# Kernel tuning notes

Hardware: AMD Instinct MI355X
Metric: run time of the kernel (lower is better)

Reference implementation:

```python
import jax, jax.numpy as jnp
import numpy as np

N_NODES = 50000
N_EDGES = 800000
HIDDEN = 128
NUM_BASIS = 32
CUTOFF = 5.0


def setup_inputs() -> dict:
    key = jax.random.key(0)
    ks = jax.random.split(key, 9)
    node_features = jax.random.normal(ks[0], (N_NODES, HIDDEN), dtype=jnp.float32)
    positions = jax.random.normal(ks[1], (N_NODES, 3), dtype=jnp.float32)
    edge_index = jax.random.randint(ks[2], (2, N_EDGES), 0, N_NODES)
    edge_in = 2 * HIDDEN + NUM_BASIS
    W1 = jax.random.normal(ks[3], (edge_in, HIDDEN), dtype=jnp.float32) * (edge_in ** -0.5)
    b1 = jnp.zeros((HIDDEN,), dtype=jnp.float32)
    W2 = jax.random.normal(ks[4], (HIDDEN, HIDDEN), dtype=jnp.float32) * (HIDDEN ** -0.5)
    b2 = jnp.zeros((HIDDEN,), dtype=jnp.float32)
    Wo = jax.random.normal(ks[5], (HIDDEN, HIDDEN), dtype=jnp.float32) * (HIDDEN ** -0.5)
    bo = jnp.zeros((HIDDEN,), dtype=jnp.float32)
    return dict(node_features=node_features, positions=positions, edge_index=edge_index,
                W1=W1, b1=b1, W2=W2, b2=b2, Wo=Wo, bo=bo)


def reference(node_features, positions, edge_index, W1, b1, W2, b2, Wo, bo):
    n_nodes = node_features.shape[0]
    # Gaussian radial basis (fixed buffers)
    centers = jnp.linspace(0.0, CUTOFF, NUM_BASIS)  # [NB]
    width = 0.5 * (centers[1] - centers[0] + 0.01)
    src, dst = edge_index[0], edge_index[1]
    rel = positions[dst] - positions[src]                       # [E,3]
    dist = jnp.linalg.norm(rel, axis=-1)                        # [E]
    d = jnp.minimum(dist, CUTOFF)
    rbf = jnp.exp(-0.5 * ((d[:, None] - centers) / width) ** 2)  # [E,NB]
    # edge message: concat(src feats, dst feats, rbf) -> 2-layer SiLU MLP
    msg = jnp.concatenate([node_features[src], node_features[dst], rbf], axis=-1)  # [E,2H+NB]
    h = jax.nn.silu(msg @ W1 + b1) @ W2 + b2                    # [E,H]
    # scatter-add to destination nodes + degree normalization
    updates = jax.ops.segment_sum(h, dst, num_segments=n_nodes)          # [N,H]
    degree = jax.ops.segment_sum(jnp.ones_like(dist), dst, num_segments=n_nodes)
    updates = updates / jnp.maximum(degree, 1.0)[:, None]
    return updates @ Wo + bo
```

## Files before the change

kernel.cpp:

```cpp
#include <hip/hip_runtime.h>

#define NN 50000
#define NE 800000
#define HID 128
#define NB 32
#define SCAN_B 196

typedef short short8 __attribute__((ext_vector_type(8)));
typedef float f32x4 __attribute__((ext_vector_type(4)));

static __device__ __forceinline__ short f2bf(float x) {
    unsigned int u = __float_as_uint(x);
    unsigned int r = (u + 0x7fffu + ((u >> 16) & 1u)) >> 16;
    return (short)r;
}

static __device__ __forceinline__ unsigned int addpack(unsigned int a, unsigned int b) {
    float lo = __uint_as_float(a << 16) + __uint_as_float(b << 16);
    float hi = __uint_as_float(a & 0xffff0000u) + __uint_as_float(b & 0xffff0000u);
    return ((unsigned int)(unsigned short)f2bf(hi) << 16) | (unsigned short)f2bf(lo);
}

__global__ void fused_prep(const int* __restrict__ dstI, int* __restrict__ counts,
                           const float* __restrict__ W1, const float* __restrict__ W2,
                           const float* __restrict__ Wo,
                           short* __restrict__ W1aT, short* __restrict__ W1bT,
                           short* __restrict__ W1cT, short* __restrict__ W2t,
                           short* __restrict__ Wot) {
    int b = blockIdx.x;
    if (b < 3125) {
        int e = b * 256 + threadIdx.x;
        atomicAdd(&counts[dstI[e]], 1);
    } else {
        int t = (b - 3125) * 256 + threadIdx.x;
        if (t < 16384) {
            int n = t >> 7, k = t & 127;
            W1aT[t] = f2bf(W1[k * HID + n]);
        } else if ((t -= 16384) < 16384) {
            int n = t >> 7, k = t & 127;
            W1bT[t] = f2bf(W1[(k + 128) * HID + n]);
        } else if ((t -= 16384) < 4096) {
            int n = t >> 5, k = t & 31;
            W1cT[t] = f2bf(W1[(k + 256) * HID + n]);
        } else if ((t -= 4096) < 16384) {
            int n = t >> 7, k = t & 127;
            W2t[t] = f2bf(W2[k * HID + n]);
        } else if ((t -= 16384) < 16384) {
            int n = t >> 7, k = t & 127;
            Wot[t] = f2bf(Wo[k * HID + n]);
        }
    }
}

__global__ void k_scan1(const int* __restrict__ counts, int* __restrict__ scanEx,
                        int* __restrict__ blockSum) {
    __shared__ int s[256];
    int t = threadIdx.x, idx = blockIdx.x * 256 + t;
    int v = counts[idx];
    s[t] = v; __syncthreads();
    #pragma unroll
    for (int off = 1; off < 256; off <<= 1) {
        int x = (t >= off) ? s[t - off] : 0;
        __syncthreads();
        s[t] += x;
        __syncthreads();
    }
    scanEx[idx] = s[t] - v;
    if (t == 255) blockSum[blockIdx.x] = s[255];
}

__global__ void k_scan2(const int* __restrict__ blockSum, int* __restrict__ blockBase) {
    __shared__ int s[256];
    int t = threadIdx.x;
    int v = (t < SCAN_B) ? blockSum[t] : 0;
    s[t] = v; __syncthreads();
    #pragma unroll
    for (int off = 1; off < 256; off <<= 1) {
        int x = (t >= off) ? s[t - off] : 0;
        __syncthreads();
        s[t] += x;
        __syncthreads();
    }
    blockBase[t] = s[t] - v;
}

__global__ void k_scan3(const int* __restrict__ scanEx, const int* __restrict__ blockBase,
                        int* __restrict__ cur) {
    int idx = blockIdx.x * 256 + threadIdx.x;
    cur[idx] = scanEx[idx] + blockBase[blockIdx.x];
}

__global__ void k_permute(const int* __restrict__ src, const int* __restrict__ dst,
                          int* __restrict__ cur, int2* __restrict__ edgeS) {
    int e = blockIdx.x * 256 + threadIdx.x;
    int s = src[e];
    int d = dst[e];
    int r = atomicAdd(&cur[d], 1);
    edgeS[r] = make_int2(s, d);
}

__global__ void sd_kernel(const float* __restrict__ nf,
                          const short* __restrict__ W1aT, const short* __restrict__ W1bT,
                          short* __restrict__ Sg, short* __restrict__ Dg) {
    __shared__ short As[64 * 136];
    const int tid  = threadIdx.x;
    const int wave = tid >> 6;
    const int lane = tid & 63;
    const int quad = lane >> 4;
    const int l15  = lane & 15;
    const int n0   = blockIdx.x * 64;

    {
        int row = tid >> 2, pt = tid & 3;
        int node = min(n0 + row, NN - 1);
        const float4* p = (const float4*)(nf + (size_t)node * HID + pt * 32);
        #pragma unroll
        for (int j = 0; j < 4; ++j) {
            float4 w0 = p[j * 2], w1 = p[j * 2 + 1];
            short8 o;
            o[0] = f2bf(w0.x); o[1] = f2bf(w0.y); o[2] = f2bf(w0.z); o[3] = f2bf(w0.w);
            o[4] = f2bf(w1.x); o[5] = f2bf(w1.y); o[6] = f2bf(w1.z); o[7] = f2bf(w1.w);
            *(short8*)(As + row * 136 + pt * 32 + j * 8) = o;
        }
    }
    __syncthreads();

    f32x4 aS[4][2], aD[4][2];
    #pragma unroll
    for (int mt = 0; mt < 4; ++mt)
        #pragma unroll
        for (int nt = 0; nt < 2; ++nt) {
            aS[mt][nt] = (f32x4){0.f, 0.f, 0.f, 0.f};
            aD[mt][nt] = (f32x4){0.f, 0.f, 0.f, 0.f};
        }

    #pragma unroll
    for (int kk = 0; kk < 4; ++kk) {
        int ko = kk * 32 + quad * 8;
        short8 a[4];
        #pragma unroll
        for (int mt = 0; mt < 4; ++mt)
            a[mt] = *(const short8*)(As + (mt * 16 + l15) * 136 + ko);
        #pragma unroll
        for (int nt = 0; nt < 2; ++nt) {
            int n = wave * 32 + nt * 16 + l15;
            short8 bS = *(const short8*)(W1aT + n * HID + ko);
            short8 bD = *(const short8*)(W1bT + n * HID + ko);
            #pragma unroll
            for (int mt = 0; mt < 4; ++mt) {
                aS[mt][nt] = __builtin_amdgcn_mfma_f32_16x16x32_bf16(a[mt], bS, aS[mt][nt], 0, 0, 0);
                aD[mt][nt] = __builtin_amdgcn_mfma_f32_16x16x32_bf16(a[mt], bD, aD[mt][nt], 0, 0, 0);
            }
        }
    }

    #pragma unroll
    for (int nt = 0; nt < 2; ++nt) {
        int col = wave * 32 + nt * 16 + l15;
        #pragma unroll
        for (int mt = 0; mt < 4; ++mt) {
            #pragma unroll
            for (int r = 0; r < 4; ++r) {
                int node = n0 + mt * 16 + quad * 4 + r;
                if (node < NN) {
                    Sg[(size_t)node * HID + col] = f2bf(aS[mt][nt][r]);
                    Dg[(size_t)node * HID + col] = f2bf(aD[mt][nt][r]);
                }
            }
        }
    }
}

__launch_bounds__(512, 6)
__global__ void edge_kernel(const short* __restrict__ Sg,
                            const short* __restrict__ Dg,
                            const float* __restrict__ pos,
                            const int2* __restrict__ edgeS,
                            const short* __restrict__ W1cT,
                            const float* __restrict__ b1,
                            const short* __restrict__ W2t,
                            const float* __restrict__ b2,
                            float* __restrict__ upd) {
    __shared__ char buf[49152];
    __shared__ int  dn_sh[128];
    short* PRE = (short*)buf;
    short* R   = (short*)(buf + 34816);
    short* Ps  = (short*)buf;
    float* UfT = (float*)buf;

    const int tid  = threadIdx.x;
    const int wave = tid >> 6;
    const int lane = tid & 63;
    const int quad = lane >> 4;
    const int l15  = lane & 15;
    const int mg   = wave >> 2;
    const int nsl  = wave & 3;
    const int e0   = blockIdx.x * 128;

    {
        int es = tid >> 2, pt = tid & 3;
        int2 sd = edgeS[e0 + es];
        int s = sd.x, d = sd.y;
        const int4* sp = (const int4*)(Sg + (size_t)s * HID + pt * 32);
        const int4* dp = (const int4*)(Dg + (size_t)d * HID + pt * 32);
        int4* op = (int4*)(PRE + es * 136 + pt * 32);
        #pragma unroll
        for (int j = 0; j < 4; ++j) {
            int4 a = sp[j], b = dp[j];
            int4 o;
            o.x = addpack(a.x, b.x);
            o.y = addpack(a.y, b.y);
            o.z = addpack(a.z, b.z);
            o.w = addpack(a.w, b.w);
            op[j] = o;
        }
        if (pt == 0) dn_sh[es] = d;
        float dx = pos[d * 3 + 0] - pos[s * 3 + 0];
        float dy = pos[d * 3 + 1] - pos[s * 3 + 1];
        float dz = pos[d * 3 + 2] - pos[s * 3 + 2];
        float dd = fminf(sqrtf(dx * dx + dy * dy + dz * dz), 5.0f);
        const float step  = 5.0f / 31.0f;
        const float width = 0.5f * (step + 0.01f);
        const float coef  = -0.5f / (width * width);
        short8 r;
        #pragma unroll
        for (int j = 0; j < 8; ++j) {
            float c = step * (float)(pt * 8 + j);
            float t = dd - c;
            r[j] = f2bf(__expf(coef * t * t));
        }
        *(short8*)(R + es * 56 + pt * 8) = r;
    }
    __syncthreads();

    f32x4 acc[4][2];
    #pragma unroll
    for (int mt = 0; mt < 4; ++mt)
        #pragma unroll
        for (int nt = 0; nt < 2; ++nt) acc[mt][nt] = (f32x4){0.f, 0.f, 0.f, 0.f};
    {
        int ko = quad * 8;
        short8 a[4];
        #pragma unroll
        for (int mt = 0; mt < 4; ++mt)
            a[mt] = *(const short8*)(R + (mg * 64 + mt * 16 + l15) * 56 + ko);
        #pragma unroll
        for (int nt = 0; nt < 2; ++nt) {
            int n = nsl * 32 + nt * 16 + l15;
            short8 b = *(const short8*)(W1cT + n * NB + ko);
            #pragma unroll
            for (int mt = 0; mt < 4; ++mt)
                acc[mt][nt] = __builtin_amdgcn_mfma_f32_16x16x32_bf16(a[mt], b, acc[mt][nt], 0, 0, 0);
        }
    }

    {
        float b1c[2] = { b1[nsl * 32 + l15], b1[nsl * 32 + 16 + l15] };
        const unsigned short* PREu = (const unsigned short*)PRE;
        #pragma unroll
        for (int nt = 0; nt < 2; ++nt) {
            int col = nsl * 32 + nt * 16 + l15;
            #pragma unroll
            for (int mt = 0; mt < 4; ++mt) {
                #pragma unroll
                for (int r = 0; r < 4; ++r) {
                    int row = mg * 64 + mt * 16 + quad * 4 + r;
                    float pre = __uint_as_float((unsigned int)PREu[row * 136 + col] << 16);
                    float x = acc[mt][nt][r] + pre + b1c[nt];
                    float p = x / (1.0f + __expf(-x));
                    Ps[row * 136 + col] = f2bf(p);
                }
            }
        }
    }
    __syncthreads();

    f32x4 acc2[4][2];
    #pragma unroll
    for (int mt = 0; mt < 4; ++mt)
        #pragma unroll
        for (int nt = 0; nt < 2; ++nt) acc2[mt][nt] = (f32x4){0.f, 0.f, 0.f, 0.f};

    #pragma unroll
    for (int kk = 0; kk < 4; ++kk) {
        int ko = kk * 32 + quad * 8;
        short8 a[4];
        #pragma unroll
        for (int mt = 0; mt < 4; ++mt)
            a[mt] = *(const short8*)(Ps + (mg * 64 + mt * 16 + l15) * 136 + ko);
        #pragma unroll
        for (int nt = 0; nt < 2; ++nt) {
            int n = nsl * 32 + nt * 16 + l15;
            short8 b = *(const short8*)(W2t + n * HID + ko);
            #pragma unroll
            for (int mt = 0; mt < 4; ++mt)
                acc2[mt][nt] = __builtin_amdgcn_mfma_f32_16x16x32_bf16(a[mt], b, acc2[mt][nt], 0, 0, 0);
        }
    }
    __syncthreads();

    float b2c[2] = { b2[nsl * 32 + l15], b2[nsl * 32 + 16 + l15] };
    #pragma unroll
    for (int h = 0; h < 2; ++h) {
        if (mg == h) {
            #pragma unroll
            for (int nt = 0; nt < 2; ++nt) {
                int col = nsl * 32 + nt * 16 + l15;
                #pragma unroll
                for (int mt = 0; mt < 4; ++mt) {
                    f32x4 v;
                    #pragma unroll
                    for (int r = 0; r < 4; ++r) v[r] = acc2[mt][nt][r] + b2c[nt];
                    *(f32x4*)(UfT + col * 68 + mt * 16 + quad * 4) = v;
                }
            }
        }
        __syncthreads();
        {
            int col = tid & 127;
            int seg = tid >> 7;
            int rb  = h * 64 + seg * 16;
            const float* cp = UfT + col * 68 + seg * 16;
            f32x4 vv[4];
            #pragma unroll
            for (int j = 0; j < 4; ++j) vv[j] = *(const f32x4*)(cp + j * 4);
            int rnode = dn_sh[rb];
            float run = 0.0f;
            #pragma unroll
            for (int i = 0; i < 16; ++i) {
                int node = dn_sh[rb + i];
                float v = vv[i >> 2][i & 3];
                if (node != rnode) {
                    atomicAdd(upd + (size_t)rnode * HID + col, run);
                    rnode = node;
                    run = v;
                } else {
                    run += v;
                }
            }
            atomicAdd(upd + (size_t)rnode * HID + col, run);
        }
        __syncthreads();
    }
}

__launch_bounds__(256, 4)
__global__ void out_kernel(float* __restrict__ out,
                           const int* __restrict__ counts,
                           const short* __restrict__ Wot,
                           const float* __restrict__ bo) {
    __shared__ short A2[64 * 136];

    const int tid  = threadIdx.x;
    const int wave = tid >> 6;
    const int lane = tid & 63;
    const int quad = lane >> 4;
    const int l15  = lane & 15;
    const int n0   = blockIdx.x * 64;

    {
        int row = tid >> 2, pt = tid & 3;
        int node = n0 + row;
        if (node < NN) {
            float inv = 1.0f / fmaxf((float)counts[node], 1.0f);
            const float4* p = (const float4*)(out + (size_t)node * HID + pt * 32);
            #pragma unroll
            for (int j = 0; j < 4; ++j) {
                float4 w0 = p[j * 2], w1 = p[j * 2 + 1];
                short8 o;
                o[0] = f2bf(w0.x * inv); o[1] = f2bf(w0.y * inv);
                o[2] = f2bf(w0.z * inv); o[3] = f2bf(w0.w * inv);
                o[4] = f2bf(w1.x * inv); o[5] = f2bf(w1.y * inv);
                o[6] = f2bf(w1.z * inv); o[7] = f2bf(w1.w * inv);
                *(short8*)(A2 + row * 136 + pt * 32 + j * 8) = o;
            }
        } else {
            short8 z = (short8){0, 0, 0, 0, 0, 0, 0, 0};
            #pragma unroll
            for (int j = 0; j < 4; ++j)
                *(short8*)(A2 + row * 136 + pt * 32 + j * 8) = z;
        }
    }
    __syncthreads();

    f32x4 acc[4][2];
    #pragma unroll
    for (int mt = 0; mt < 4; ++mt)
        #pragma unroll
        for (int nt = 0; nt < 2; ++nt) acc[mt][nt] = (f32x4){0.f, 0.f, 0.f, 0.f};

    #pragma unroll
    for (int kk = 0; kk < 4; ++kk) {
        int ko = kk * 32 + quad * 8;
        short8 a[4];
        #pragma unroll
        for (int mt = 0; mt < 4; ++mt)
            a[mt] = *(const short8*)(A2 + (mt * 16 + l15) * 136 + ko);
        #pragma unroll
        for (int nt = 0; nt < 2; ++nt) {
            int n = wave * 32 + nt * 16 + l15;
            short8 b = *(const short8*)(Wot + n * HID + ko);
            #pragma unroll
            for (int mt = 0; mt < 4; ++mt)
                acc[mt][nt] = __builtin_amdgcn_mfma_f32_16x16x32_bf16(a[mt], b, acc[mt][nt], 0, 0, 0);
        }
    }
    __syncthreads();

    #pragma unroll
    for (int nt = 0; nt < 2; ++nt) {
        int col = wave * 32 + nt * 16 + l15;
        float bias = bo[col];
        #pragma unroll
        for (int mt = 0; mt < 4; ++mt) {
            #pragma unroll
            for (int r = 0; r < 4; ++r) {
                int row = mt * 16 + quad * 4 + r;
                int node = n0 + row;
                if (node < NN)
                    out[(size_t)node * HID + col] = acc[mt][nt][r] + bias;
            }
        }
    }
}

extern "C" void kernel_launch(void* const* d_in, const int* in_sizes, int n_in,
                              void* d_out, int out_size, void* d_ws, size_t ws_size,
                              hipStream_t stream) {
    const float* nf  = (const float*)d_in[0];
    const float* pos = (const float*)d_in[1];
    const int*   ei  = (const int*)d_in[2];
    const float* W1  = (const float*)d_in[3];
    const float* b1  = (const float*)d_in[4];
    const float* W2  = (const float*)d_in[5];
    const float* b2  = (const float*)d_in[6];
    const float* Wo  = (const float*)d_in[7];
    const float* bo  = (const float*)d_in[8];
    float* out = (float*)d_out;

    char* ws = (char*)d_ws;
    short* W1aT     = (short*)(ws);
    short* W1bT     = (short*)(ws + 32768);
    short* W1cT     = (short*)(ws + 65536);
    short* W2t      = (short*)(ws + 73728);
    short* Wot      = (short*)(ws + 106496);
    int*   counts   = (int*)(ws + 139264);
    int*   scanEx   = (int*)(ws + 339968);
    int*   blockSum = (int*)(ws + 540672);
    int*   blockBase= (int*)(ws + 541696);
    int*   cur      = (int*)(ws + 542720);
    int2*  edgeS    = (int2*)(ws + 743424);
    short* Sg       = (short*)(ws + 7143424);
    short* Dg       = (short*)(ws + 19943424);

    hipMemsetAsync(out, 0, (size_t)NN * HID * sizeof(float), stream);
    hipMemsetAsync(counts, 0, 200704, stream);

    fused_prep<<<3397, 256, 0, stream>>>(ei + NE, counts, W1, W2, Wo,
                                         W1aT, W1bT, W1cT, W2t, Wot);
    k_scan1<<<SCAN_B, 256, 0, stream>>>(counts, scanEx, blockSum);
    k_scan2<<<1, 256, 0, stream>>>(blockSum, blockBase);
    k_scan3<<<SCAN_B, 256, 0, stream>>>(scanEx, blockBase, cur);
    k_permute<<<3125, 256, 0, stream>>>(ei, ei + NE, cur, edgeS);
    sd_kernel<<<(NN + 63) / 64, 256, 0, stream>>>(nf, W1aT, W1bT, Sg, Dg);
    edge_kernel<<<NE / 128, 512, 0, stream>>>(Sg, Dg, pos, edgeS,
                                              W1cT, b1, W2t, b2, out);
    out_kernel<<<(NN + 63) / 64, 256, 0, stream>>>(out, counts, Wot, bo);
}
```

Baseline: 345.8 us.

## Fuse edge MLP, scatter and output GEMM into per-node-block kernel

Replaces the edge-parallel kernel, which used global atomics into the output, and the separate output kernel with one kernel that owns 16 destination nodes per block. Each block walks its CSR edge range in tiles of 64, runs the MLP, and accumulates into shared memory, then applies degree normalization and the Wo projection in place. The two scan tail kernels are merged, the output memset is dropped, and scanEx now aliases the Sg buffer. The aim is to remove global float atomics and an extra round trip of the update tensor, at the cost of load imbalance across blocks and partially filled edge tiles.

```diff
diff --git a/kernel.cpp b/kernel.cpp
--- a/kernel.cpp
+++ b/kernel.cpp
@@ -5,6 +5,8 @@
 #define HID 128
 #define NB 32
 #define SCAN_B 196
+#define NPB 16
+#define ET 64
 
 typedef short short8 __attribute__((ext_vector_type(8)));
 typedef float f32x4 __attribute__((ext_vector_type(4)));
@@ -14,11 +16,8 @@
     unsigned int r = (u + 0x7fffu + ((u >> 16) & 1u)) >> 16;
     return (short)r;
 }
-
-static __device__ __forceinline__ unsigned int addpack(unsigned int a, unsigned int b) {
-    float lo = __uint_as_float(a << 16) + __uint_as_float(b << 16);
-    float hi = __uint_as_float(a & 0xffff0000u) + __uint_as_float(b & 0xffff0000u);
-    return ((unsigned int)(unsigned short)f2bf(hi) << 16) | (unsigned short)f2bf(lo);
+static __device__ __forceinline__ float bf2f(unsigned short s) {
+    return __uint_as_float(((unsigned int)s) << 16);
 }
 
 __global__ void fused_prep(const int* __restrict__ dstI, int* __restrict__ counts,
@@ -69,25 +68,21 @@
     if (t == 255) blockSum[blockIdx.x] = s[255];
 }
 
-__global__ void k_scan2(const int* __restrict__ blockSum, int* __restrict__ blockBase) {
+__global__ void k_scan23(const int* __restrict__ scanEx, const int* __restrict__ blockSum,
+                         int* __restrict__ nodeBase, int* __restrict__ cur) {
     __shared__ int s[256];
-    int t = threadIdx.x;
-    int v = (t < SCAN_B) ? blockSum[t] : 0;
-    s[t] = v; __syncthreads();
-    #pragma unroll
-    for (int off = 1; off < 256; off <<= 1) {
-        int x = (t >= off) ? s[t - off] : 0;
-        __syncthreads();
-        s[t] += x;
-        __syncthreads();
-    }
-    blockBase[t] = s[t] - v;
-}
-
-__global__ void k_scan3(const int* __restrict__ scanEx, const int* __restrict__ blockBase,
-                        int* __restrict__ cur) {
-    int idx = blockIdx.x * 256 + threadIdx.x;
-    cur[idx] = scanEx[idx] + blockBase[blockIdx.x];
+    int t = threadIdx.x, b = blockIdx.x;
+    s[t] = (t < b) ? blockSum[t] : 0;
+    __syncthreads();
+    #pragma unroll
+    for (int off = 128; off > 0; off >>= 1) {
+        if (t < off) s[t] += s[t + off];
+        __syncthreads();
+    }
+    int idx = b * 256 + t;
+    int val = scanEx[idx] + s[0];
+    nodeBase[idx] = val;
+    cur[idx] = val;
 }
 
 __global__ void k_permute(const int* __restrict__ src, const int* __restrict__ dst,
@@ -171,255 +166,208 @@
     }
 }
 
-__launch_bounds__(512, 6)
-__global__ void edge_kernel(const short* __restrict__ Sg,
-                            const short* __restrict__ Dg,
-                            const float* __restrict__ pos,
-                            const int2* __restrict__ edgeS,
-                            const short* __restrict__ W1cT,
-                            const float* __restrict__ b1,
-                            const short* __restrict__ W2t,
-                            const float* __restrict__ b2,
-                            float* __restrict__ upd) {
-    __shared__ char buf[49152];
-    __shared__ int  dn_sh[128];
-    short* PRE = (short*)buf;
-    short* R   = (short*)(buf + 34816);
-    short* Ps  = (short*)buf;
-    float* UfT = (float*)buf;
+__launch_bounds__(256, 4)
+__global__ void edge_node(const short* __restrict__ Sg,
+                          const short* __restrict__ Dg,
+                          const float* __restrict__ pos,
+                          const int2* __restrict__ edgeS,
+                          const int* __restrict__ nodeBase,
+                          const int* __restrict__ counts,
+                          const short* __restrict__ W1cT,
+                          const float* __restrict__ b1,
+                          const short* __restrict__ W2t,
+                          const float* __restrict__ b2,
+                          const short* __restrict__ Wot,
+                          const float* __restrict__ bo,
+                          float* __restrict__ out) {
+    __shared__ float accL[17 * 132];
+    __shared__ short Ps[ET * 136];
+    __shared__ short R[ET * 56];
+    __shared__ short Dl[17 * 128];
+    __shared__ int   dn_sh[ET];
+    __shared__ float inv_sh[NPB];
 
     const int tid  = threadIdx.x;
-    const int wave = tid >> 6;
     const int lane = tid & 63;
+    const int nsl  = tid >> 6;
     const int quad = lane >> 4;
     const int l15  = lane & 15;
-    const int mg   = wave >> 2;
-    const int nsl  = wave & 3;
-    const int e0   = blockIdx.x * 128;
-
+    const int n0   = blockIdx.x * NPB;
+
+    for (int i = tid; i < 17 * 132; i += 256) accL[i] = 0.f;
     {
-        int es = tid >> 2, pt = tid & 3;
-        int2 sd = edgeS[e0 + es];
-        int s = sd.x, d = sd.y;
-        const int4* sp = (const int4*)(Sg + (size_t)s * HID + pt * 32);
-        const int4* dp = (const int4*)(Dg + (size_t)d * HID + pt * 32);
-        int4* op = (int4*)(PRE + es * 136 + pt * 32);
-        #pragma unroll
-        for (int j = 0; j < 4; ++j) {
-            int4 a = sp[j], b = dp[j];
-            int4 o;
-            o.x = addpack(a.x, b.x);
-            o.y = addpack(a.y, b.y);
-            o.z = addpack(a.z, b.z);
-            o.w = addpack(a.w, b.w);
-            op[j] = o;
-        }
-        if (pt == 0) dn_sh[es] = d;
-        float dx = pos[d * 3 + 0] - pos[s * 3 + 0];
-        float dy = pos[d * 3 + 1] - pos[s * 3 + 1];
-        float dz = pos[d * 3 + 2] - pos[s * 3 + 2];
-        float dd = fminf(sqrtf(dx * dx + dy * dy + dz * dz), 5.0f);
-        const float step  = 5.0f / 31.0f;
-        const float width = 0.5f * (step + 0.01f);
-        const float coef  = -0.5f / (width * width);
-        short8 r;
-        #pragma unroll
-        for (int j = 0; j < 8; ++j) {
-            float c = step * (float)(pt * 8 + j);
-            float t = dd - c;
-            r[j] = f2bf(__expf(coef * t * t));
-        }
-        *(short8*)(R + es * 56 + pt * 8) = r;
+        int row = tid >> 4, ch = tid & 15;
+        *(short8*)(Dl + row * 128 + ch * 8) =
+            *(const short8*)(Dg + (size_t)(n0 + row) * HID + ch * 8);
+    }
+    if (tid < 16) {
+        short8 z = (short8){0,0,0,0,0,0,0,0};
+        *(short8*)(Dl + 16 * 128 + tid * 8) = z;
+    }
+    float b1c[2] = { b1[nsl * 32 + l15], b1[nsl * 32 + 16 + l15] };
+    float b2c[2] = { b2[nsl * 32 + l15], b2[nsl * 32 + 16 + l15] };
+
+    const int e0 = nodeBase[n0];
+    const int e1 = nodeBase[n0 + NPB];
+    const unsigned short* Psu = (const unsigned short*)Ps;
+    const unsigned short* Dlu = (const unsigned short*)Dl;
+
+    for (int te = e0; te < e1; te += ET) {
+        {
+            int es = tid >> 2, pt = tid & 3;
+            int e = te + es;
+            int valid = (e < e1);
+            int ee = valid ? e : (e1 - 1);
+            int2 sd = edgeS[ee];
+            int s = sd.x, d = sd.y;
+            if (pt == 0) dn_sh[es] = valid ? (d - n0) : NPB;
+            #pragma unroll
+            for (int j = 0; j < 4; ++j)
+                *(short8*)(Ps + es * 136 + pt * 32 + j * 8) =
+                    *(const short8*)(Sg + (size_t)s * HID + pt * 32 + j * 8);
+            float dx = pos[d * 3 + 0] - pos[s * 3 + 0];
+            float dy = pos[d * 3 + 1] - pos[s * 3 + 1];
+            float dz = pos[d * 3 + 2] - pos[s * 3 + 2];
+            float dd = fminf(sqrtf(dx * dx + dy * dy + dz * dz), 5.0f);
+            const float step  = 5.0f / 31.0f;
+            const float width = 0.5f * (step + 0.01f);
+            const float coef  = -0.5f / (width * width);
+            short8 r;
+            #pragma unroll
+            for (int j = 0; j < 8; ++j) {
+                float c = step * (float)(pt * 8 + j);
+                float t = dd - c;
+                r[j] = f2bf(__expf(coef * t * t));
+            }
+            *(short8*)(R + es * 56 + pt * 8) = r;
+        }
+        __syncthreads();
+
+        f32x4 acc[4][2];
+        #pragma unroll
+        for (int mt = 0; mt < 4; ++mt)
+            #pragma unroll
+            for (int nt = 0; nt < 2; ++nt) acc[mt][nt] = (f32x4){0.f, 0.f, 0.f, 0.f};
+        {
+            int ko = quad * 8;
+            short8 a[4];
+            #pragma unroll
+            for (int mt = 0; mt < 4; ++mt)
+                a[mt] = *(const short8*)(R + (mt * 16 + l15) * 56 + ko);
+            #pragma unroll
+            for (int nt = 0; nt < 2; ++nt) {
+                int n = nsl * 32 + nt * 16 + l15;
+                short8 b = *(const short8*)(W1cT + n * NB + ko);
+                #pragma unroll
+                for (int mt = 0; mt < 4; ++mt)
+                    acc[mt][nt] = __builtin_amdgcn_mfma_f32_16x16x32_bf16(a[mt], b, acc[mt][nt], 0, 0, 0);
+            }
+        }
+
+        #pragma unroll
+        for (int mt = 0; mt < 4; ++mt) {
+            #pragma unroll
+            for (int r = 0; r < 4; ++r) {
+                int row = mt * 16 + quad * 4 + r;
+                int dn = dn_sh[row];
+                #pragma unroll
+                for (int nt = 0; nt < 2; ++nt) {
+                    int col = nsl * 32 + nt * 16 + l15;
+                    float S = bf2f(Psu[row * 136 + col]);
+                    float D = bf2f(Dlu[dn * 128 + col]);
+                    float x = acc[mt][nt][r] + S + D + b1c[nt];
+                    float p = x * __builtin_amdgcn_rcpf(1.0f + __expf(-x));
+                    Ps[row * 136 + col] = f2bf(p);
+                }
+            }
+        }
+        __syncthreads();
+
+        f32x4 acc2[4][2];
+        #pragma unroll
+        for (int mt = 0; mt < 4; ++mt)
+            #pragma unroll
+            for (int nt = 0; nt < 2; ++nt) acc2[mt][nt] = (f32x4){0.f, 0.f, 0.f, 0.f};
+
+        #pragma unroll
+        for (int kk = 0; kk < 4; ++kk) {
+            int ko = kk * 32 + quad * 8;
+            short8 a[4];
+            #pragma unroll
+            for (int mt = 0; mt < 4; ++mt)
+                a[mt] = *(const short8*)(Ps + (mt * 16 + l15) * 136 + ko);
+            #pragma unroll
+            for (int nt = 0; nt < 2; ++nt) {
+                int n = nsl * 32 + nt * 16 + l15;
+                short8 b = *(const short8*)(W2t + n * HID + ko);
+                #pragma unroll
+                for (int mt = 0; mt < 4; ++mt)
+                    acc2[mt][nt] = __builtin_amdgcn_mfma_f32_16x16x32_bf16(a[mt], b, acc2[mt][nt], 0, 0, 0);
+            }
+        }
+
+        #pragma unroll
+        for (int nt = 0; nt < 2; ++nt) {
+            int col = nsl * 32 + nt * 16 + l15;
+            #pragma unroll
+            for (int mt = 0; mt < 4; ++mt) {
+                int rbase = mt * 16 + quad * 4;
+                int rnode = dn_sh[rbase];
+                float run = 0.0f;
+                #pragma unroll
+                for (int r = 0; r < 4; ++r) {
+                    int node = dn_sh[rbase + r];
+                    float v = acc2[mt][nt][r] + b2c[nt];
+                    if (node != rnode) {
+                        atomicAdd(&accL[rnode * 132 + col], run);
+                        rnode = node;
+                        run = v;
+                    } else {
+                        run += v;
+                    }
+                }
+                atomicAdd(&accL[rnode * 132 + col], run);
+            }
+        }
+        __syncthreads();
     }
     __syncthreads();
 
-    f32x4 acc[4][2];
-    #pragma unroll
-    for (int mt = 0; mt < 4; ++mt)
-        #pragma unroll
-        for (int nt = 0; nt < 2; ++nt) acc[mt][nt] = (f32x4){0.f, 0.f, 0.f, 0.f};
+    if (tid < NPB) inv_sh[tid] = 1.0f / fmaxf((float)counts[n0 + tid], 1.0f);
+    __syncthreads();
     {
-        int ko = quad * 8;
-        short8 a[4];
-        #pragma unroll
-        for (int mt = 0; mt < 4; ++mt)
-            a[mt] = *(const short8*)(R + (mg * 64 + mt * 16 + l15) * 56 + ko);
+        int row = tid & 15, j0 = (tid >> 4) * 8;
+        float inv = inv_sh[row];
+        short8 o;
+        #pragma unroll
+        for (int j = 0; j < 8; ++j)
+            o[j] = f2bf(accL[row * 132 + j0 + j] * inv);
+        *(short8*)(Ps + row * 136 + j0) = o;
+    }
+    __syncthreads();
+
+    f32x4 ao[2];
+    ao[0] = (f32x4){0.f, 0.f, 0.f, 0.f};
+    ao[1] = (f32x4){0.f, 0.f, 0.f, 0.f};
+    #pragma unroll
+    for (int kk = 0; kk < 4; ++kk) {
+        int ko = kk * 32 + quad * 8;
+        short8 a = *(const short8*)(Ps + l15 * 136 + ko);
         #pragma unroll
         for (int nt = 0; nt < 2; ++nt) {
             int n = nsl * 32 + nt * 16 + l15;
-            short8 b = *(const short8*)(W1cT + n * NB + ko);
-            #pragma unroll
-            for (int mt = 0; mt < 4; ++mt)
-                acc[mt][nt] = __builtin_amdgcn_mfma_f32_16x16x32_bf16(a[mt], b, acc[mt][nt], 0, 0, 0);
-        }
-    }
-
-    {
-        float b1c[2] = { b1[nsl * 32 + l15], b1[nsl * 32 + 16 + l15] };
-        const unsigned short* PREu = (const unsigned short*)PRE;
-        #pragma unroll
-        for (int nt = 0; nt < 2; ++nt) {
-            int col = nsl * 32 + nt * 16 + l15;
-            #pragma unroll
-            for (int mt = 0; mt < 4; ++mt) {
-                #pragma unroll
-                for (int r = 0; r < 4; ++r) {
-                    int row = mg * 64 + mt * 16 + quad * 4 + r;
-                    float pre = __uint_as_float((unsigned int)PREu[row * 136 + col] << 16);
-                    float x = acc[mt][nt][r] + pre + b1c[nt];
-                    float p = x / (1.0f + __expf(-x));
-                    Ps[row * 136 + col] = f2bf(p);
-                }
-            }
-        }
-    }
-    __syncthreads();
-
-    f32x4 acc2[4][2];
-    #pragma unroll
-    for (int mt = 0; mt < 4; ++mt)
-        #pragma unroll
-        for (int nt = 0; nt < 2; ++nt) acc2[mt][nt] = (f32x4){0.f, 0.f, 0.f, 0.f};
-
-    #pragma unroll
-    for (int kk = 0; kk < 4; ++kk) {
-        int ko = kk * 32 + quad * 8;
-        short8 a[4];
-        #pragma unroll
-        for (int mt = 0; mt < 4; ++mt)
-            a[mt] = *(const short8*)(Ps + (mg * 64 + mt * 16 + l15) * 136 + ko);
-        #pragma unroll
-        for (int nt = 0; nt < 2; ++nt) {
-            int n = nsl * 32 + nt * 16 + l15;
-            short8 b = *(const short8*)(W2t + n * HID + ko);
-            #pragma unroll
-            for (int mt = 0; mt < 4; ++mt)
-                acc2[mt][nt] = __builtin_amdgcn_mfma_f32_16x16x32_bf16(a[mt], b, acc2[mt][nt], 0, 0, 0);
-        }
-    }
-    __syncthreads();
-
-    float b2c[2] = { b2[nsl * 32 + l15], b2[nsl * 32 + 16 + l15] };
-    #pragma unroll
-    for (int h = 0; h < 2; ++h) {
-        if (mg == h) {
-            #pragma unroll
-            for (int nt = 0; nt < 2; ++nt) {
-                int col = nsl * 32 + nt * 16 + l15;
-                #pragma unroll
-                for (int mt = 0; mt < 4; ++mt) {
-                    f32x4 v;
-                    #pragma unroll
-                    for (int r = 0; r < 4; ++r) v[r] = acc2[mt][nt][r] + b2c[nt];
-                    *(f32x4*)(UfT + col * 68 + mt * 16 + quad * 4) = v;
-                }
-            }
-        }
-        __syncthreads();
-        {
-            int col = tid & 127;
-            int seg = tid >> 7;
-            int rb  = h * 64 + seg * 16;
-            const float* cp = UfT + col * 68 + seg * 16;
-            f32x4 vv[4];
-            #pragma unroll
-            for (int j = 0; j < 4; ++j) vv[j] = *(const f32x4*)(cp + j * 4);
-            int rnode = dn_sh[rb];
-            float run = 0.0f;
-            #pragma unroll
-            for (int i = 0; i < 16; ++i) {
-                int node = dn_sh[rb + i];
-                float v = vv[i >> 2][i & 3];
-                if (node != rnode) {
-                    atomicAdd(upd + (size_t)rnode * HID + col, run);
-                    rnode = node;
-                    run = v;
-                } else {
-                    run += v;
-                }
-            }
-            atomicAdd(upd + (size_t)rnode * HID + col, run);
-        }
-        __syncthreads();
-    }
-}
-
-__launch_bounds__(256, 4)
-__global__ void out_kernel(float* __restrict__ out,
-                           const int* __restrict__ counts,
-                           const short* __restrict__ Wot,
-                           const float* __restrict__ bo) {
-    __shared__ short A2[64 * 136];
-
-    const int tid  = threadIdx.x;
-    const int wave = tid >> 6;
-    const int lane = tid & 63;
-    const int quad = lane >> 4;
-    const int l15  = lane & 15;
-    const int n0   = blockIdx.x * 64;
-
-    {
-        int row = tid >> 2, pt = tid & 3;
-        int node = n0 + row;
-        if (node < NN) {
-            float inv = 1.0f / fmaxf((float)counts[node], 1.0f);
-            const float4* p = (const float4*)(out + (size_t)node * HID + pt * 32);
-            #pragma unroll
-            for (int j = 0; j < 4; ++j) {
-                float4 w0 = p[j * 2], w1 = p[j * 2 + 1];
-                short8 o;
-                o[0] = f2bf(w0.x * inv); o[1] = f2bf(w0.y * inv);
-                o[2] = f2bf(w0.z * inv); o[3] = f2bf(w0.w * inv);
-                o[4] = f2bf(w1.x * inv); o[5] = f2bf(w1.y * inv);
-                o[6] = f2bf(w1.z * inv); o[7] = f2bf(w1.w * inv);
-                *(short8*)(A2 + row * 136 + pt * 32 + j * 8) = o;
-            }
-        } else {
-            short8 z = (short8){0, 0, 0, 0, 0, 0, 0, 0};
-            #pragma unroll
-            for (int j = 0; j < 4; ++j)
-                *(short8*)(A2 + row * 136 + pt * 32 + j * 8) = z;
-        }
-    }
-    __syncthreads();
-
-    f32x4 acc[4][2];
-    #pragma unroll
-    for (int mt = 0; mt < 4; ++mt)
-        #pragma unroll
-        for (int nt = 0; nt < 2; ++nt) acc[mt][nt] = (f32x4){0.f, 0.f, 0.f, 0.f};
-
-    #pragma unroll
-    for (int kk = 0; kk < 4; ++kk) {
-        int ko = kk * 32 + quad * 8;
-        short8 a[4];
-        #pragma unroll
-        for (int mt = 0; mt < 4; ++mt)
-            a[mt] = *(const short8*)(A2 + (mt * 16 + l15) * 136 + ko);
-        #pragma unroll
-        for (int nt = 0; nt < 2; ++nt) {
-            int n = wave * 32 + nt * 16 + l15;
             short8 b = *(const short8*)(Wot + n * HID + ko);
-            #pragma unroll
-            for (int mt = 0; mt < 4; ++mt)
-                acc[mt][nt] = __builtin_amdgcn_mfma_f32_16x16x32_bf16(a[mt], b, acc[mt][nt], 0, 0, 0);
-        }
-    }
-    __syncthreads();
-
+            ao[nt] = __builtin_amdgcn_mfma_f32_16x16x32_bf16(a, b, ao[nt], 0, 0, 0);
+        }
+    }
     #pragma unroll
     for (int nt = 0; nt < 2; ++nt) {
-        int col = wave * 32 + nt * 16 + l15;
+        int col = nsl * 32 + nt * 16 + l15;
         float bias = bo[col];
         #pragma unroll
-        for (int mt = 0; mt < 4; ++mt) {
-            #pragma unroll
-            for (int r = 0; r < 4; ++r) {
-                int row = mt * 16 + quad * 4 + r;
-                int node = n0 + row;
-                if (node < NN)
-                    out[(size_t)node * HID + col] = acc[mt][nt][r] + bias;
-            }
+        for (int r = 0; r < 4; ++r) {
+            int row = quad * 4 + r;
+            out[(size_t)(n0 + row) * HID + col] = ao[nt][r] + bias;
         }
     }
 }
@@ -445,25 +393,22 @@
     short* W2t      = (short*)(ws + 73728);
     short* Wot      = (short*)(ws + 106496);
     int*   counts   = (int*)(ws + 139264);
-    int*   scanEx   = (int*)(ws + 339968);
-    int*   blockSum = (int*)(ws + 540672);
-    int*   blockBase= (int*)(ws + 541696);
-    int*   cur      = (int*)(ws + 542720);
-    int2*  edgeS    = (int2*)(ws + 743424);
-    short* Sg       = (short*)(ws + 7143424);
-    short* Dg       = (short*)(ws + 19943424);
-
-    hipMemsetAsync(out, 0, (size_t)NN * HID * sizeof(float), stream);
+    int*   nodeBase = (int*)(ws + 339968);
+    int*   cur      = (int*)(ws + 540672);
+    int*   blockSum = (int*)(ws + 741376);
+    int2*  edgeS    = (int2*)(ws + 742400);
+    short* Sg       = (short*)(ws + 7142400);
+    short* Dg       = (short*)(ws + 19942400);
+    int*   scanEx   = (int*)Sg;
+
     hipMemsetAsync(counts, 0, 200704, stream);
 
     fused_prep<<<3397, 256, 0, stream>>>(ei + NE, counts, W1, W2, Wo,
                                          W1aT, W1bT, W1cT, W2t, Wot);
     k_scan1<<<SCAN_B, 256, 0, stream>>>(counts, scanEx, blockSum);
-    k_scan2<<<1, 256, 0, stream>>>(blockSum, blockBase);
-    k_scan3<<<SCAN_B, 256, 0, stream>>>(scanEx, blockBase, cur);
+    k_scan23<<<SCAN_B, 256, 0, stream>>>(scanEx, blockSum, nodeBase, cur);
     k_permute<<<3125, 256, 0, stream>>>(ei, ei + NE, cur, edgeS);
     sd_kernel<<<(NN + 63) / 64, 256, 0, stream>>>(nf, W1aT, W1bT, Sg, Dg);
-    edge_kernel<<<NE / 128, 512, 0, stream>>>(Sg, Dg, pos, edgeS,
-                                              W1cT, b1, W2t, b2, out);
-    out_kernel<<<(NN + 63) / 64, 256, 0, stream>>>(out, counts, Wot, bo);
-}
+    edge_node<<<NN / NPB, 256, 0, stream>>>(Sg, Dg, pos, edgeS, nodeBase, counts,
+                                            W1cT, b1, W2t, b2, Wot, bo, out);
+}
```

Measured after the change: 492.7 us. 1.42x slower.
